# Optimization experiments

Measured on AMD Instinct MI355X. Metric: run time of the kernel, lower is better.

## Reference

```python
import jax, jax.numpy as jnp
import numpy as np

WINDOW = 7
SHIFT = 3
HEADS = 4


def _rel_pos_index(w):
    # same construction as ShiftedWindowAttention.__init__ (numpy, static)
    coords = np.stack(np.meshgrid(np.arange(w), np.arange(w), indexing='ij'))  # [2,w,w]
    cf = coords.reshape(2, -1)                       # [2, w*w]
    rc = (cf[:, :, None] - cf[:, None, :]).transpose(1, 2, 0)  # [L,L,2]
    rc[:, :, 0] += w - 1
    rc[:, :, 1] += w - 1
    rc[:, :, 0] *= 2 * w - 1
    return rc.sum(-1).reshape(-1)                    # [L*L]


def _attn_mask(H, W, w, s):
    # cyclic-shift attention mask, static numpy constant
    m = np.zeros((H, W))
    slices = ((0, -w), (-w, -s), (-s, None))
    cnt = 0
    for hs in slices:
        for ws in slices:
            m[hs[0]:hs[1], ws[0]:ws[1]] = cnt
            cnt += 1
    m = m.reshape(H // w, w, W // w, w).transpose(0, 2, 1, 3).reshape(-1, w * w)  # [nwin, L]
    d = m[:, None, :] - m[:, :, None]                # [nwin, L, L]
    return np.where(d != 0, -100.0, 0.0).astype(np.float32)


def setup_inputs() -> dict:
    key = jax.random.key(0)
    ks = jax.random.split(key, 6)
    B, H, W, C = 64, 56, 56, 128
    return {
        'x': jax.random.normal(ks[0], (B, H, W, C), dtype=jnp.float32),
        'qkv_weight': jax.random.normal(ks[1], (3 * C, C), dtype=jnp.float32) * 0.02,
        'qkv_bias': jax.random.normal(ks[2], (3 * C,), dtype=jnp.float32) * 0.02,
        'proj_weight': jax.random.normal(ks[3], (C, C), dtype=jnp.float32) * 0.02,
        'proj_bias': jax.random.normal(ks[4], (C,), dtype=jnp.float32) * 0.02,
        'rel_bias_table': jax.random.normal(ks[5], ((2 * WINDOW - 1) ** 2, HEADS), dtype=jnp.float32) * 0.02,
    }


def reference(x, qkv_weight, qkv_bias, proj_weight, proj_bias, rel_bias_table):
    B, H, W, C = x.shape
    w, s, h = WINDOW, SHIFT, HEADS
    d = C // h
    nH, nW = H // w, W // w
    nwin = nH * nW
    L = w * w

    # relative position bias: [h, L, L]
    bias = rel_bias_table[jnp.asarray(_rel_pos_index(w))].reshape(L, L, h).transpose(2, 0, 1)

    # cyclic shift + window partition -> [B*nwin, L, C]
    xs = jnp.roll(x, (-s, -s), axis=(1, 2))
    xw = xs.reshape(B, nH, w, nW, w, C).transpose(0, 1, 3, 2, 4, 5).reshape(B * nwin, L, C)

    # fused qkv projection (F.linear: x @ W.T + b)
    qkv = (xw @ qkv_weight.T + qkv_bias).reshape(B * nwin, L, 3, h, d).transpose(2, 0, 3, 1, 4)
    q, k, v = qkv[0] * (d ** -0.5), qkv[1], qkv[2]   # each [B*nwin, h, L, d]

    attn = jnp.einsum('nhqd,nhkd->nhqk', q, k) + bias[None]
    mask = jnp.asarray(_attn_mask(H, W, w, s))       # [nwin, L, L]
    attn = attn.reshape(B, nwin, h, L, L) + mask[None, :, None]
    attn = jax.nn.softmax(attn.reshape(B * nwin, h, L, L), axis=-1)

    out = jnp.einsum('nhqk,nhkd->nhqd', attn, v).transpose(0, 2, 1, 3).reshape(B * nwin, L, C)
    out = out @ proj_weight.T + proj_bias

    # window merge + reverse shift -> [B, H, W, C]
    out = out.reshape(B, nH, nW, w, w, C).transpose(0, 1, 3, 2, 4, 5).reshape(B, H, W, C)
    return jnp.roll(out, (s, s), axis=(1, 2))
```

## Files before the change

### kernel.cpp

```cpp
#include <hip/hip_runtime.h>

typedef __attribute__((ext_vector_type(8))) short short8;
typedef __attribute__((ext_vector_type(4))) float f32x4;

static __device__ __forceinline__ unsigned short f2bf(float f) {
  union { float f; unsigned int u; } v; v.f = f;
  unsigned int r = v.u + 0x7FFFu + ((v.u >> 16) & 1u);
  return (unsigned short)(r >> 16);
}
static __device__ __forceinline__ unsigned int pack2(float a, float b) {
  return (unsigned int)f2bf(a) | ((unsigned int)f2bf(b) << 16);
}

#define KO 0
#define VO 2560
#define PO 4864
#define TO 7424
#define WSTRIDE 7776

__global__ __launch_bounds__(256) void k_prep(const float* __restrict__ wq,
    const float* __restrict__ wp, unsigned short* __restrict__ dq,
    unsigned short* __restrict__ dp) {
  int i = blockIdx.x * 256 + threadIdx.x;
  if (i < 384 * 128) dq[i] = f2bf(wq[i]);
  if (i < 128 * 128) dp[i] = f2bf(wp[i]);
}

static __device__ __forceinline__ int reg3(int y) { return y < 49 ? 0 : (y < 53 ? 1 : 2); }

__global__ __launch_bounds__(256, 2) void k_fused(const float* __restrict__ x,
    const unsigned short* __restrict__ Wq, const float* __restrict__ qb,
    const unsigned short* __restrict__ Wp, const float* __restrict__ pb,
    const float* __restrict__ table, float* __restrict__ out) {
  __shared__ __align__(16) unsigned short lds[4 * WSTRIDE];
  const int tid = threadIdx.x;
  const int win = blockIdx.x;
  const int b = win >> 6, wl = win & 63;
  const int wh = wl >> 3, ww = wl & 7;
  const int wv = tid >> 6, ln = tid & 63;
  const int l15 = ln & 15, l4 = ln >> 4;
  unsigned short* W = lds + wv * WSTRIDE;
  float* tblw = (float*)&W[TO];

  for (int i = ln; i < 169; i += 64) tblw[i] = table[i * 4 + wv];

  const float* rp[4];
  int vld[4];
#pragma unroll
  for (int mt = 0; mt < 4; ++mt) {
    const int t = mt * 16 + l15;
    vld[mt] = (t < 49);
    int th = t / 7, tw = t - th * 7;
    int sh = wh * 7 + th + 3; if (sh >= 56) sh -= 56;
    int sw = ww * 7 + tw + 3; if (sw >= 56) sw -= 56;
    rp[mt] = x + (((size_t)(b * 56 + (vld[mt] ? sh : 0))) * 56 + (vld[mt] ? sw : 0)) * 128;
  }
  int nrow[6];
#pragma unroll
  for (int j = 0; j < 6; ++j) {
    const int grp = j >> 1, sub = j & 1;
    nrow[j] = grp * 128 + wv * 32 + sub * 16 + l15;
  }

  const f32x4 z4 = {0.f, 0.f, 0.f, 0.f};
  f32x4 acc[4][6];
#pragma unroll
  for (int mt = 0; mt < 4; ++mt)
#pragma unroll
    for (int j = 0; j < 6; ++j) acc[mt][j] = z4;
#pragma unroll
  for (int ks = 0; ks < 4; ++ks) {
    short8 af[4], bf[6];
#pragma unroll
    for (int mt = 0; mt < 4; ++mt) {
      if (vld[mt]) {
        const float4* p = (const float4*)(rp[mt] + ks * 32 + l4 * 8);
        float4 fa = p[0], fb = p[1];
        uint4 u;
        u.x = pack2(fa.x, fa.y); u.y = pack2(fa.z, fa.w);
        u.z = pack2(fb.x, fb.y); u.w = pack2(fb.z, fb.w);
        af[mt] = *(short8*)&u;
      } else {
        const uint4 u = {0u, 0u, 0u, 0u};
        af[mt] = *(short8*)&u;
      }
    }
#pragma unroll
    for (int j = 0; j < 6; ++j)
      bf[j] = *(const short8*)&Wq[(size_t)nrow[j] * 128 + ks * 32 + l4 * 8];
#pragma unroll
    for (int mt = 0; mt < 4; ++mt)
#pragma unroll
      for (int j = 0; j < 6; ++j)
        acc[mt][j] = __builtin_amdgcn_mfma_f32_16x16x32_bf16(af[mt], bf[j], acc[mt][j], 0, 0, 0);
  }
#pragma unroll
  for (int j = 0; j < 6; ++j) {
    const float bb = qb[nrow[j]];
    const int grp = j >> 1, sub = j & 1;
#pragma unroll
    for (int mt = 0; mt < 4; ++mt)
#pragma unroll
      for (int r = 0; r < 4; ++r) {
        const int t = mt * 16 + l4 * 4 + r;
        const float v = acc[mt][j][r] + bb;
        if (grp == 0)      W[PO + t * 40 + sub * 16 + l15] = f2bf(v * 0.17677669529663687f);
        else if (grp == 1) W[KO + t * 40 + sub * 16 + l15] = f2bf(v);
        else               W[VO + (sub * 16 + l15) * 72 + t] = f2bf(v);
      }
  }
  short8 qf[4], kf[4];
#pragma unroll
  for (int mt = 0; mt < 4; ++mt)
    qf[mt] = *(const short8*)&W[PO + (mt * 16 + l15) * 40 + l4 * 8];
#pragma unroll
  for (int nt = 0; nt < 4; ++nt)
    kf[nt] = *(const short8*)&W[KO + (nt * 16 + l15) * 40 + l4 * 8];
  f32x4 s[4][4];
#pragma unroll
  for (int mt = 0; mt < 4; ++mt)
#pragma unroll
    for (int nt = 0; nt < 4; ++nt) s[mt][nt] = z4;
#pragma unroll
  for (int mt = 0; mt < 4; ++mt)
#pragma unroll
    for (int nt = 0; nt < 4; ++nt)
      s[mt][nt] = __builtin_amdgcn_mfma_f32_16x16x32_bf16(qf[mt], kf[nt], s[mt][nt], 0, 0, 0);

  int jh_[4], jw_[4], jreg[4], jj[4];
#pragma unroll
  for (int nt = 0; nt < 4; ++nt) {
    const int j = nt * 16 + l15;
    jj[nt] = j;
    const int jh = j / 7, jw = j - jh * 7;
    jh_[nt] = jh; jw_[nt] = jw;
    jreg[nt] = 3 * reg3(wh * 7 + jh) + reg3(ww * 7 + jw);
  }
  float est2[16], est3[16];
#pragma unroll
  for (int mt = 0; mt < 4; ++mt) {
#pragma unroll
    for (int r = 0; r < 4; ++r) {
      const int i = mt * 16 + l4 * 4 + r;
      const int ih = i / 7, iw = i - ih * 7;
      const int ireg = 3 * reg3(wh * 7 + ih) + reg3(ww * 7 + iw);
      float e[4];
      float mx = -1e30f;
#pragma unroll
      for (int nt = 0; nt < 4; ++nt) {
        int didx = (ih - jh_[nt] + 6) * 13 + (iw - jw_[nt] + 6);
        didx = didx < 0 ? 0 : (didx > 168 ? 168 : didx);
        float v = s[mt][nt][r] + tblw[didx];
        if (ireg != jreg[nt]) v -= 100.0f;
        if (jj[nt] >= 49) v = -1e30f;
        e[nt] = v;
        mx = fmaxf(mx, v);
      }
#pragma unroll
      for (int off = 1; off < 16; off <<= 1) mx = fmaxf(mx, __shfl_xor(mx, off, 16));
      float sum = 0.0f;
#pragma unroll
      for (int nt = 0; nt < 4; ++nt) {
        float ev = (e[nt] > -1e29f) ? __expf(e[nt] - mx) : 0.0f;
        e[nt] = ev; sum += ev;
      }
#pragma unroll
      for (int off = 1; off < 16; off <<= 1) sum += __shfl_xor(sum, off, 16);
      const float inv = 1.0f / sum;
      if (i < 49) {
        W[PO + i * 40 + l15]      = f2bf(e[0] * inv);
        W[PO + i * 40 + 16 + l15] = f2bf(e[1] * inv);
      }
      est2[mt * 4 + r] = e[2] * inv;
      est3[mt * 4 + r] = e[3] * inv;
    }
  }
  f32x4 o[4][2];
#pragma unroll
  for (int mt = 0; mt < 4; ++mt)
#pragma unroll
    for (int dt = 0; dt < 2; ++dt) o[mt][dt] = z4;
  {
    short8 pa[4], vb[2];
#pragma unroll
    for (int mt = 0; mt < 4; ++mt)
      pa[mt] = *(const short8*)&W[PO + (mt * 16 + l15) * 40 + l4 * 8];
#pragma unroll
    for (int dt = 0; dt < 2; ++dt)
      vb[dt] = *(const short8*)&W[VO + (dt * 16 + l15) * 72 + l4 * 8];
#pragma unroll
    for (int mt = 0; mt < 4; ++mt)
#pragma unroll
      for (int dt = 0; dt < 2; ++dt)
        o[mt][dt] = __builtin_amdgcn_mfma_f32_16x16x32_bf16(pa[mt], vb[dt], o[mt][dt], 0, 0, 0);
  }
#pragma unroll
  for (int mt = 0; mt < 4; ++mt)
#pragma unroll
    for (int r = 0; r < 4; ++r) {
      const int i = mt * 16 + l4 * 4 + r;
      if (i < 49) {
        W[PO + i * 40 + l15]      = f2bf(est2[mt * 4 + r]);
        W[PO + i * 40 + 16 + l15] = f2bf(est3[mt * 4 + r]);
      }
    }
  {
    short8 pa[4], vb[2];
#pragma unroll
    for (int mt = 0; mt < 4; ++mt)
      pa[mt] = *(const short8*)&W[PO + (mt * 16 + l15) * 40 + l4 * 8];
#pragma unroll
    for (int dt = 0; dt < 2; ++dt)
      vb[dt] = *(const short8*)&W[VO + (dt * 16 + l15) * 72 + 32 + l4 * 8];
#pragma unroll
    for (int mt = 0; mt < 4; ++mt)
#pragma unroll
      for (int dt = 0; dt < 2; ++dt)
        o[mt][dt] = __builtin_amdgcn_mfma_f32_16x16x32_bf16(pa[mt], vb[dt], o[mt][dt], 0, 0, 0);
  }
#pragma unroll
  for (int mt = 0; mt < 4; ++mt)
#pragma unroll
    for (int dt = 0; dt < 2; ++dt)
#pragma unroll
      for (int r = 0; r < 4; ++r)
        W[KO + (mt * 16 + l4 * 4 + r) * 40 + dt * 16 + l15] = f2bf(o[mt][dt][r]);

  __syncthreads();

  f32x4 c2[4][2];
#pragma unroll
  for (int mt = 0; mt < 4; ++mt)
#pragma unroll
    for (int nt = 0; nt < 2; ++nt) c2[mt][nt] = z4;
#pragma unroll
  for (int ks = 0; ks < 4; ++ks) {
    short8 af[4], bp[2];
#pragma unroll
    for (int mt = 0; mt < 4; ++mt)
      af[mt] = *(const short8*)&lds[ks * WSTRIDE + KO + (mt * 16 + l15) * 40 + l4 * 8];
#pragma unroll
    for (int nt = 0; nt < 2; ++nt)
      bp[nt] = *(const short8*)&Wp[(size_t)(wv * 32 + nt * 16 + l15) * 128 + ks * 32 + l4 * 8];
#pragma unroll
    for (int mt = 0; mt < 4; ++mt)
#pragma unroll
      for (int nt = 0; nt < 2; ++nt)
        c2[mt][nt] = __builtin_amdgcn_mfma_f32_16x16x32_bf16(af[mt], bp[nt], c2[mt][nt], 0, 0, 0);
  }
#pragma unroll
  for (int mt = 0; mt < 4; ++mt) {
#pragma unroll
    for (int r = 0; r < 4; ++r) {
      const int t = mt * 16 + l4 * 4 + r;
      if (t < 49) {
        const int th = t / 7, tw = t - th * 7;
        int y = wh * 7 + th + 3; if (y >= 56) y -= 56;
        int xx = ww * 7 + tw + 3; if (xx >= 56) xx -= 56;
        float* dstp = out + (((size_t)(b * 56 + y)) * 56 + xx) * 128;
#pragma unroll
        for (int nt = 0; nt < 2; ++nt) {
          const int n = wv * 32 + nt * 16 + l15;
          dstp[n] = c2[mt][nt][r] + pb[n];
        }
      }
    }
  }
}

extern "C" void kernel_launch(void* const* d_in, const int* in_sizes, int n_in,
                              void* d_out, int out_size, void* d_ws, size_t ws_size,
                              hipStream_t stream) {
  const float* x     = (const float*)d_in[0];
  const float* qkvw  = (const float*)d_in[1];
  const float* qkvb  = (const float*)d_in[2];
  const float* projw = (const float*)d_in[3];
  const float* projb = (const float*)d_in[4];
  const float* table = (const float*)d_in[5];
  float* out = (float*)d_out;
  char* ws = (char*)d_ws;
  unsigned short* Wq = (unsigned short*)ws;
  unsigned short* Wp = (unsigned short*)(ws + 98304);

  k_prep<<<dim3(192), dim3(256), 0, stream>>>(qkvw, projw, Wq, Wp);
  k_fused<<<dim3(4096), dim3(256), 0, stream>>>(x, Wq, qkvb, Wp, projb, table, out);
}
```

Measured before the change: 164.0 us.

## Swap MFMA operands to get transposed accumulators for vectorized stores and row softmax

Swaps the A/B operands of the QK, PV, projection and Q/K-projection MFMAs so each lane's accumulator holds four consecutive columns of one row. This lets LDS writes of Q, K, probabilities and attention output use packed 64-bit stores, and lets the final output use float4 global stores instead of scalar ones. Softmax now reduces within a lane first, then needs only two cross-lane shuffles instead of four per row. Invalid-row loads are clamped to a valid address and masked by select instead of branching. The layout changes bring some risk of index errors and extra register pressure.

```diff
diff --git a/kernel.cpp b/kernel.cpp
--- a/kernel.cpp
+++ b/kernel.cpp
@@ -12,9 +12,9 @@
   return (unsigned int)f2bf(a) | ((unsigned int)f2bf(b) << 16);
 }
 
-#define KO 0
-#define VO 2560
-#define PO 4864
+#define QO 0
+#define KO 2560
+#define VO 5120
 #define TO 7424
 #define WSTRIDE 7776
 
@@ -45,146 +45,184 @@
   for (int i = ln; i < 169; i += 64) tblw[i] = table[i * 4 + wv];
 
   const float* rp[4];
-  int vld[4];
+  bool vld[4];
 #pragma unroll
   for (int mt = 0; mt < 4; ++mt) {
     const int t = mt * 16 + l15;
     vld[mt] = (t < 49);
-    int th = t / 7, tw = t - th * 7;
+    const int tc = vld[mt] ? t : 0;
+    const int th = tc / 7, tw = tc - th * 7;
     int sh = wh * 7 + th + 3; if (sh >= 56) sh -= 56;
     int sw = ww * 7 + tw + 3; if (sw >= 56) sw -= 56;
-    rp[mt] = x + (((size_t)(b * 56 + (vld[mt] ? sh : 0))) * 56 + (vld[mt] ? sw : 0)) * 128;
+    rp[mt] = x + (((size_t)(b * 56 + sh)) * 56 + sw) * 128;
   }
   int nrow[6];
 #pragma unroll
-  for (int j = 0; j < 6; ++j) {
-    const int grp = j >> 1, sub = j & 1;
-    nrow[j] = grp * 128 + wv * 32 + sub * 16 + l15;
-  }
+  for (int j = 0; j < 6; ++j)
+    nrow[j] = (j >> 1) * 128 + wv * 32 + (j & 1) * 16 + l15;
 
   const f32x4 z4 = {0.f, 0.f, 0.f, 0.f};
-  f32x4 acc[4][6];
-#pragma unroll
-  for (int mt = 0; mt < 4; ++mt)
-#pragma unroll
-    for (int j = 0; j < 6; ++j) acc[mt][j] = z4;
+  f32x4 aS[4][4], aV[4][2];
+#pragma unroll
+  for (int mt = 0; mt < 4; ++mt) {
+#pragma unroll
+    for (int j = 0; j < 4; ++j) aS[mt][j] = z4;
+#pragma unroll
+    for (int j = 0; j < 2; ++j) aV[mt][j] = z4;
+  }
 #pragma unroll
   for (int ks = 0; ks < 4; ++ks) {
     short8 af[4], bf[6];
 #pragma unroll
     for (int mt = 0; mt < 4; ++mt) {
-      if (vld[mt]) {
-        const float4* p = (const float4*)(rp[mt] + ks * 32 + l4 * 8);
-        float4 fa = p[0], fb = p[1];
-        uint4 u;
-        u.x = pack2(fa.x, fa.y); u.y = pack2(fa.z, fa.w);
-        u.z = pack2(fb.x, fb.y); u.w = pack2(fb.z, fb.w);
-        af[mt] = *(short8*)&u;
-      } else {
-        const uint4 u = {0u, 0u, 0u, 0u};
-        af[mt] = *(short8*)&u;
-      }
+      const float4* p = (const float4*)(rp[mt] + ks * 32 + l4 * 8);
+      float4 fa = p[0], fb = p[1];
+      uint4 u;
+      u.x = pack2(fa.x, fa.y); u.y = pack2(fa.z, fa.w);
+      u.z = pack2(fb.x, fb.y); u.w = pack2(fb.z, fb.w);
+      u.x = vld[mt] ? u.x : 0u; u.y = vld[mt] ? u.y : 0u;
+      u.z = vld[mt] ? u.z : 0u; u.w = vld[mt] ? u.w : 0u;
+      af[mt] = *(short8*)&u;
     }
 #pragma unroll
     for (int j = 0; j < 6; ++j)
       bf[j] = *(const short8*)&Wq[(size_t)nrow[j] * 128 + ks * 32 + l4 * 8];
 #pragma unroll
-    for (int mt = 0; mt < 4; ++mt)
-#pragma unroll
-      for (int j = 0; j < 6; ++j)
-        acc[mt][j] = __builtin_amdgcn_mfma_f32_16x16x32_bf16(af[mt], bf[j], acc[mt][j], 0, 0, 0);
-  }
-#pragma unroll
-  for (int j = 0; j < 6; ++j) {
-    const float bb = qb[nrow[j]];
-    const int grp = j >> 1, sub = j & 1;
-#pragma unroll
-    for (int mt = 0; mt < 4; ++mt)
-#pragma unroll
-      for (int r = 0; r < 4; ++r) {
-        const int t = mt * 16 + l4 * 4 + r;
-        const float v = acc[mt][j][r] + bb;
-        if (grp == 0)      W[PO + t * 40 + sub * 16 + l15] = f2bf(v * 0.17677669529663687f);
-        else if (grp == 1) W[KO + t * 40 + sub * 16 + l15] = f2bf(v);
-        else               W[VO + (sub * 16 + l15) * 72 + t] = f2bf(v);
-      }
-  }
-  short8 qf[4], kf[4];
+    for (int mt = 0; mt < 4; ++mt) {
+#pragma unroll
+      for (int j = 0; j < 4; ++j)
+        aS[mt][j] = __builtin_amdgcn_mfma_f32_16x16x32_bf16(bf[j], af[mt], aS[mt][j], 0, 0, 0);
+#pragma unroll
+      for (int j = 0; j < 2; ++j)
+        aV[mt][j] = __builtin_amdgcn_mfma_f32_16x16x32_bf16(af[mt], bf[4 + j], aV[mt][j], 0, 0, 0);
+    }
+  }
+  {
+    const float SC = 0.17677669529663687f;
+    const float4 bq0 = *(const float4*)(qb + wv * 32 + 4 * l4);
+    const float4 bq1 = *(const float4*)(qb + wv * 32 + 16 + 4 * l4);
+    const float4 bk0 = *(const float4*)(qb + 128 + wv * 32 + 4 * l4);
+    const float4 bk1 = *(const float4*)(qb + 128 + wv * 32 + 16 + 4 * l4);
+    const float bv0 = qb[256 + wv * 32 + l15];
+    const float bv1 = qb[256 + wv * 32 + 16 + l15];
+#pragma unroll
+    for (int mt = 0; mt < 4; ++mt) {
+      const int t = mt * 16 + l15;
+      uint2 u;
+      u.x = pack2((aS[mt][0][0] + bq0.x) * SC, (aS[mt][0][1] + bq0.y) * SC);
+      u.y = pack2((aS[mt][0][2] + bq0.z) * SC, (aS[mt][0][3] + bq0.w) * SC);
+      *(uint2*)&W[QO + t * 40 + 4 * l4] = u;
+      u.x = pack2((aS[mt][1][0] + bq1.x) * SC, (aS[mt][1][1] + bq1.y) * SC);
+      u.y = pack2((aS[mt][1][2] + bq1.z) * SC, (aS[mt][1][3] + bq1.w) * SC);
+      *(uint2*)&W[QO + t * 40 + 16 + 4 * l4] = u;
+      u.x = pack2(aS[mt][2][0] + bk0.x, aS[mt][2][1] + bk0.y);
+      u.y = pack2(aS[mt][2][2] + bk0.z, aS[mt][2][3] + bk0.w);
+      *(uint2*)&W[KO + t * 40 + 4 * l4] = u;
+      u.x = pack2(aS[mt][3][0] + bk1.x, aS[mt][3][1] + bk1.y);
+      u.y = pack2(aS[mt][3][2] + bk1.z, aS[mt][3][3] + bk1.w);
+      *(uint2*)&W[KO + t * 40 + 16 + 4 * l4] = u;
+      u.x = pack2(aV[mt][0][0] + bv0, aV[mt][0][1] + bv0);
+      u.y = pack2(aV[mt][0][2] + bv0, aV[mt][0][3] + bv0);
+      *(uint2*)&W[VO + l15 * 72 + mt * 16 + 4 * l4] = u;
+      u.x = pack2(aV[mt][1][0] + bv1, aV[mt][1][1] + bv1);
+      u.y = pack2(aV[mt][1][2] + bv1, aV[mt][1][3] + bv1);
+      *(uint2*)&W[VO + (16 + l15) * 72 + mt * 16 + 4 * l4] = u;
+    }
+  }
+
+  f32x4 s[4][4];
 #pragma unroll
   for (int mt = 0; mt < 4; ++mt)
-    qf[mt] = *(const short8*)&W[PO + (mt * 16 + l15) * 40 + l4 * 8];
-#pragma unroll
-  for (int nt = 0; nt < 4; ++nt)
-    kf[nt] = *(const short8*)&W[KO + (nt * 16 + l15) * 40 + l4 * 8];
-  f32x4 s[4][4];
-#pragma unroll
-  for (int mt = 0; mt < 4; ++mt)
 #pragma unroll
     for (int nt = 0; nt < 4; ++nt) s[mt][nt] = z4;
-#pragma unroll
-  for (int mt = 0; mt < 4; ++mt)
+  {
+    short8 qf[4], kf[4];
+#pragma unroll
+    for (int mt = 0; mt < 4; ++mt)
+      qf[mt] = *(const short8*)&W[QO + (mt * 16 + l15) * 40 + l4 * 8];
 #pragma unroll
     for (int nt = 0; nt < 4; ++nt)
-      s[mt][nt] = __builtin_amdgcn_mfma_f32_16x16x32_bf16(qf[mt], kf[nt], s[mt][nt], 0, 0, 0);
-
-  int jh_[4], jw_[4], jreg[4], jj[4];
+      kf[nt] = *(const short8*)&W[KO + (nt * 16 + l15) * 40 + l4 * 8];
+#pragma unroll
+    for (int mt = 0; mt < 4; ++mt)
+#pragma unroll
+      for (int nt = 0; nt < 4; ++nt)
+        s[mt][nt] = __builtin_amdgcn_mfma_f32_16x16x32_bf16(kf[nt], qf[mt], s[mt][nt], 0, 0, 0);
+  }
+
+  int ih4[4], iw4[4], irg[4];
+#pragma unroll
+  for (int mt = 0; mt < 4; ++mt) {
+    const int i = mt * 16 + l15;
+    const int ihh = i / 7, iww = i - ihh * 7;
+    ih4[mt] = ihh; iw4[mt] = iww;
+    irg[mt] = 3 * reg3(wh * 7 + ihh) + reg3(ww * 7 + iww);
+  }
+  float pmax[4] = {-1e30f, -1e30f, -1e30f, -1e30f};
 #pragma unroll
   for (int nt = 0; nt < 4; ++nt) {
-    const int j = nt * 16 + l15;
-    jj[nt] = j;
-    const int jh = j / 7, jw = j - jh * 7;
-    jh_[nt] = jh; jw_[nt] = jw;
-    jreg[nt] = 3 * reg3(wh * 7 + jh) + reg3(ww * 7 + jw);
-  }
-  float est2[16], est3[16];
-#pragma unroll
-  for (int mt = 0; mt < 4; ++mt) {
 #pragma unroll
     for (int r = 0; r < 4; ++r) {
-      const int i = mt * 16 + l4 * 4 + r;
-      const int ih = i / 7, iw = i - ih * 7;
-      const int ireg = 3 * reg3(wh * 7 + ih) + reg3(ww * 7 + iw);
-      float e[4];
-      float mx = -1e30f;
-#pragma unroll
-      for (int nt = 0; nt < 4; ++nt) {
-        int didx = (ih - jh_[nt] + 6) * 13 + (iw - jw_[nt] + 6);
+      const int j = nt * 16 + 4 * l4 + r;
+      const int jhh = j / 7, jww = j - jhh * 7;
+      const int jrg = 3 * reg3(wh * 7 + jhh) + reg3(ww * 7 + jww);
+      const bool jbad = (j >= 49);
+#pragma unroll
+      for (int mt = 0; mt < 4; ++mt) {
+        int didx = (ih4[mt] - jhh + 6) * 13 + (iw4[mt] - jww + 6);
         didx = didx < 0 ? 0 : (didx > 168 ? 168 : didx);
         float v = s[mt][nt][r] + tblw[didx];
-        if (ireg != jreg[nt]) v -= 100.0f;
-        if (jj[nt] >= 49) v = -1e30f;
-        e[nt] = v;
-        mx = fmaxf(mx, v);
+        if (irg[mt] != jrg) v -= 100.0f;
+        if (jbad) v = -1e30f;
+        s[mt][nt][r] = v;
+        pmax[mt] = fmaxf(pmax[mt], v);
       }
-#pragma unroll
-      for (int off = 1; off < 16; off <<= 1) mx = fmaxf(mx, __shfl_xor(mx, off, 16));
-      float sum = 0.0f;
-#pragma unroll
-      for (int nt = 0; nt < 4; ++nt) {
-        float ev = (e[nt] > -1e29f) ? __expf(e[nt] - mx) : 0.0f;
-        e[nt] = ev; sum += ev;
+    }
+  }
+  float inv[4];
+#pragma unroll
+  for (int mt = 0; mt < 4; ++mt) {
+    float m0 = pmax[mt];
+    m0 = fmaxf(m0, __shfl_xor(m0, 16));
+    m0 = fmaxf(m0, __shfl_xor(m0, 32));
+    float sum = 0.0f;
+#pragma unroll
+    for (int nt = 0; nt < 4; ++nt)
+#pragma unroll
+      for (int r = 0; r < 4; ++r) {
+        const float v = s[mt][nt][r];
+        const float e = (v > -1e29f) ? __expf(v - m0) : 0.0f;
+        s[mt][nt][r] = e;
+        sum += e;
       }
-#pragma unroll
-      for (int off = 1; off < 16; off <<= 1) sum += __shfl_xor(sum, off, 16);
-      const float inv = 1.0f / sum;
-      if (i < 49) {
-        W[PO + i * 40 + l15]      = f2bf(e[0] * inv);
-        W[PO + i * 40 + 16 + l15] = f2bf(e[1] * inv);
+    sum += __shfl_xor(sum, 16);
+    sum += __shfl_xor(sum, 32);
+    inv[mt] = 1.0f / sum;
+  }
+
+  f32x4 o[4][2];
+#pragma unroll
+  for (int mt = 0; mt < 4; ++mt)
+#pragma unroll
+    for (int dt = 0; dt < 2; ++dt) o[mt][dt] = z4;
+#pragma unroll
+  for (int mt = 0; mt < 4; ++mt) {
+    const int i = mt * 16 + l15;
+    if (i < 49) {
+#pragma unroll
+      for (int nt = 0; nt < 2; ++nt) {
+        uint2 u;
+        u.x = pack2(s[mt][nt][0] * inv[mt], s[mt][nt][1] * inv[mt]);
+        u.y = pack2(s[mt][nt][2] * inv[mt], s[mt][nt][3] * inv[mt]);
+        *(uint2*)&W[QO + i * 40 + nt * 16 + 4 * l4] = u;
       }
-      est2[mt * 4 + r] = e[2] * inv;
-      est3[mt * 4 + r] = e[3] * inv;
-    }
-  }
-  f32x4 o[4][2];
-#pragma unroll
-  for (int mt = 0; mt < 4; ++mt)
-#pragma unroll
-    for (int dt = 0; dt < 2; ++dt) o[mt][dt] = z4;
+    }
+  }
   {
     short8 pa[4], vb[2];
 #pragma unroll
     for (int mt = 0; mt < 4; ++mt)
-      pa[mt] = *(const short8*)&W[PO + (mt * 16 + l15) * 40 + l4 * 8];
+      pa[mt] = *(const short8*)&W[QO + (mt * 16 + l15) * 40 + l4 * 8];
 #pragma unroll
     for (int dt = 0; dt < 2; ++dt)
       vb[dt] = *(const short8*)&W[VO + (dt * 16 + l15) * 72 + l4 * 8];
@@ -192,23 +230,26 @@
     for (int mt = 0; mt < 4; ++mt)
 #pragma unroll
       for (int dt = 0; dt < 2; ++dt)
-        o[mt][dt] = __builtin_amdgcn_mfma_f32_16x16x32_bf16(pa[mt], vb[dt], o[mt][dt], 0, 0, 0);
-  }
-#pragma unroll
-  for (int mt = 0; mt < 4; ++mt)
-#pragma unroll
-    for (int r = 0; r < 4; ++r) {
-      const int i = mt * 16 + l4 * 4 + r;
-      if (i < 49) {
-        W[PO + i * 40 + l15]      = f2bf(est2[mt * 4 + r]);
-        W[PO + i * 40 + 16 + l15] = f2bf(est3[mt * 4 + r]);
+        o[mt][dt] = __builtin_amdgcn_mfma_f32_16x16x32_bf16(vb[dt], pa[mt], o[mt][dt], 0, 0, 0);
+  }
+#pragma unroll
+  for (int mt = 0; mt < 4; ++mt) {
+    const int i = mt * 16 + l15;
+    if (i < 49) {
+#pragma unroll
+      for (int nt = 2; nt < 4; ++nt) {
+        uint2 u;
+        u.x = pack2(s[mt][nt][0] * inv[mt], s[mt][nt][1] * inv[mt]);
+        u.y = pack2(s[mt][nt][2] * inv[mt], s[mt][nt][3] * inv[mt]);
+        *(uint2*)&W[QO + i * 40 + (nt - 2) * 16 + 4 * l4] = u;
       }
     }
+  }
   {
     short8 pa[4], vb[2];
 #pragma unroll
     for (int mt = 0; mt < 4; ++mt)
-      pa[mt] = *(const short8*)&W[PO + (mt * 16 + l15) * 40 + l4 * 8];
+      pa[mt] = *(const short8*)&W[QO + (mt * 16 + l15) * 40 + l4 * 8];
 #pragma unroll
     for (int dt = 0; dt < 2; ++dt)
       vb[dt] = *(const short8*)&W[VO + (dt * 16 + l15) * 72 + 32 + l4 * 8];
@@ -216,29 +257,34 @@
     for (int mt = 0; mt < 4; ++mt)
 #pragma unroll
       for (int dt = 0; dt < 2; ++dt)
-        o[mt][dt] = __builtin_amdgcn_mfma_f32_16x16x32_bf16(pa[mt], vb[dt], o[mt][dt], 0, 0, 0);
-  }
+        o[mt][dt] = __builtin_amdgcn_mfma_f32_16x16x32_bf16(vb[dt], pa[mt], o[mt][dt], 0, 0, 0);
+  }
+#pragma unroll
+  for (int mt = 0; mt < 4; ++mt) {
+    const int t = mt * 16 + l15;
+#pragma unroll
+    for (int dt = 0; dt < 2; ++dt) {
+      uint2 u;
+      u.x = pack2(o[mt][dt][0], o[mt][dt][1]);
+      u.y = pack2(o[mt][dt][2], o[mt][dt][3]);
+      *(uint2*)&W[KO + t * 40 + dt * 16 + 4 * l4] = u;
+    }
+  }
+  __syncthreads();
+
+  const float4 pbv0 = *(const float4*)(pb + wv * 32 + 4 * l4);
+  const float4 pbv1 = *(const float4*)(pb + wv * 32 + 16 + 4 * l4);
+  f32x4 c2[4][2];
 #pragma unroll
   for (int mt = 0; mt < 4; ++mt)
 #pragma unroll
-    for (int dt = 0; dt < 2; ++dt)
-#pragma unroll
-      for (int r = 0; r < 4; ++r)
-        W[KO + (mt * 16 + l4 * 4 + r) * 40 + dt * 16 + l15] = f2bf(o[mt][dt][r]);
-
-  __syncthreads();
-
-  f32x4 c2[4][2];
-#pragma unroll
-  for (int mt = 0; mt < 4; ++mt)
-#pragma unroll
     for (int nt = 0; nt < 2; ++nt) c2[mt][nt] = z4;
 #pragma unroll
   for (int ks = 0; ks < 4; ++ks) {
-    short8 af[4], bp[2];
-#pragma unroll
-    for (int mt = 0; mt < 4; ++mt)
-      af[mt] = *(const short8*)&lds[ks * WSTRIDE + KO + (mt * 16 + l15) * 40 + l4 * 8];
+    short8 a2[4], bp[2];
+#pragma unroll
+    for (int mt = 0; mt < 4; ++mt)
+      a2[mt] = *(const short8*)&lds[ks * WSTRIDE + KO + (mt * 16 + l15) * 40 + l4 * 8];
 #pragma unroll
     for (int nt = 0; nt < 2; ++nt)
       bp[nt] = *(const short8*)&Wp[(size_t)(wv * 32 + nt * 16 + l15) * 128 + ks * 32 + l4 * 8];
@@ -246,24 +292,23 @@
     for (int mt = 0; mt < 4; ++mt)
 #pragma unroll
       for (int nt = 0; nt < 2; ++nt)
-        c2[mt][nt] = __builtin_amdgcn_mfma_f32_16x16x32_bf16(af[mt], bp[nt], c2[mt][nt], 0, 0, 0);
-  }
-#pragma unroll
-  for (int mt = 0; mt < 4; ++mt) {
-#pragma unroll
-    for (int r = 0; r < 4; ++r) {
-      const int t = mt * 16 + l4 * 4 + r;
-      if (t < 49) {
-        const int th = t / 7, tw = t - th * 7;
-        int y = wh * 7 + th + 3; if (y >= 56) y -= 56;
-        int xx = ww * 7 + tw + 3; if (xx >= 56) xx -= 56;
-        float* dstp = out + (((size_t)(b * 56 + y)) * 56 + xx) * 128;
-#pragma unroll
-        for (int nt = 0; nt < 2; ++nt) {
-          const int n = wv * 32 + nt * 16 + l15;
-          dstp[n] = c2[mt][nt][r] + pb[n];
-        }
-      }
+        c2[mt][nt] = __builtin_amdgcn_mfma_f32_16x16x32_bf16(bp[nt], a2[mt], c2[mt][nt], 0, 0, 0);
+  }
+#pragma unroll
+  for (int mt = 0; mt < 4; ++mt) {
+    const int t = mt * 16 + l15;
+    if (t < 49) {
+      const int th = t / 7, tw = t - th * 7;
+      int y = wh * 7 + th + 3; if (y >= 56) y -= 56;
+      int xx = ww * 7 + tw + 3; if (xx >= 56) xx -= 56;
+      float* dstp = out + (((size_t)(b * 56 + y)) * 56 + xx) * 128 + wv * 32 + 4 * l4;
+      float4 v0, v1;
+      v0.x = c2[mt][0][0] + pbv0.x; v0.y = c2[mt][0][1] + pbv0.y;
+      v0.z = c2[mt][0][2] + pbv0.z; v0.w = c2[mt][0][3] + pbv0.w;
+      *(float4*)(dstp) = v0;
+      v1.x = c2[mt][1][0] + pbv1.x; v1.y = c2[mt][1][1] + pbv1.y;
+      v1.z = c2[mt][1][2] + pbv1.z; v1.w = c2[mt][1][3] + pbv1.w;
+      *(float4*)(dstp + 16) = v1;
     }
   }
 }
```

Result: faster. 154.0 us (-6.1%).
